# Performance work log

Measured on AMD Instinct MI355X. Metric: run time of the kernel, lower is better.

The kernel has to match this reference:

```python
import jax, jax.numpy as jnp
import numpy as np

EPS = 1e-8


def _conv1(x, w):
    # x: [C,H,W], w: [O,C,k,k] -> [O,H,W] (SAME padding, stride 1)
    return jax.lax.conv_general_dilated(
        x[None], w, window_strides=(1, 1), padding='SAME',
        dimension_numbers=('NCHW', 'OIHW', 'NCHW'))[0]


def setup_inputs() -> dict:
    key = jax.random.key(0)
    k1, k2, k3, k4 = jax.random.split(key, 4)
    B, C, O, K, S, H, W = 8, 512, 512, 3, 512, 64, 64
    inp = jax.random.normal(k1, (B, C, H, W), dtype=jnp.float32)
    style = jax.random.normal(k2, (B, S), dtype=jnp.float32)
    weight = jax.random.normal(k3, (1, O, C, K, K), dtype=jnp.float32)  # conv weight
    mod_weight = jax.random.normal(k4, (C, S), dtype=jnp.float32)      # EqualLinear weight
    mod_bias = jnp.ones((C,), dtype=jnp.float32)                        # bias filled with 1.0
    return {"input": inp, "style": style, "weight": weight,
            "mod_weight": mod_weight, "mod_bias": mod_bias}


def reference(input, style, weight, mod_weight, mod_bias) -> jnp.ndarray:
    B, C, H, W = input.shape
    _, O, _, K, _ = weight.shape
    fan_in = C * K * K
    scale = 1.0 / np.sqrt(fan_in)
    lin_scale = 1.0 / np.sqrt(mod_weight.shape[1])

    # EqualLinear modulation: [B, C]
    s = style @ (mod_weight * lin_scale).T + mod_bias

    # Modulate + demodulate per-sample weights: [B, O, C, K, K]
    w = scale * weight * s[:, None, :, None, None]
    demod = jax.lax.rsqrt(jnp.sum(w * w, axis=(2, 3, 4)) + EPS)  # [B, O]
    w = w * demod[:, :, None, None, None]

    # Grouped conv with groups=B == per-sample conv, vmapped over batch
    out = jax.vmap(_conv1)(input, w)  # [B, O, H, W]
    return out
```

## Files before the change

kernel.cpp:

```cpp
#include <hip/hip_runtime.h>

typedef unsigned short u16;
typedef __bf16 bf16_t;
typedef bf16_t bf16x8 __attribute__((ext_vector_type(8)));
typedef float floatx4 __attribute__((ext_vector_type(4)));

static constexpr float kScale = 0.014731391274719741f;
static constexpr float kScale2 = 2.1701388888888894e-4f;
static constexpr float kLinScale = 0.044194173824159216f;

__device__ __forceinline__ u16 f2bf(float f) {
  unsigned u = __float_as_uint(f);
  u += 0x7FFFu + ((u >> 16) & 1u);
  return (u16)(u >> 16);
}

#define GLD16(g, l)                                                        \
  __builtin_amdgcn_global_load_lds(                                        \
      (const __attribute__((address_space(1))) unsigned int*)(g),          \
      (__attribute__((address_space(3))) unsigned int*)(l), 16, 0, 0)

__global__ __launch_bounds__(256) void k_prep1(const float* __restrict__ style,
                                               const float* __restrict__ modw,
                                               const float* __restrict__ modb,
                                               const float* __restrict__ weight,
                                               float* __restrict__ s_buf,
                                               float* __restrict__ ssq) {
  int tid = threadIdx.x;
  if (blockIdx.x < 1024) {
    int lane = tid & 63, wv = tid >> 6;
    int idx = blockIdx.x * 4 + wv;
    int b = idx >> 9, c = idx & 511;
    const float* st = style + b * 512;
    const float* mw = modw + (size_t)c * 512;
    float s = 0.f;
#pragma unroll
    for (int i = 0; i < 8; ++i) s += st[lane + i * 64] * mw[lane + i * 64];
#pragma unroll
    for (int off = 32; off; off >>= 1) s += __shfl_xor(s, off);
    if (lane == 0) s_buf[idx] = s * kLinScale + modb[c];
  } else {
    int e = (blockIdx.x - 1024) * 256 + tid;
    const float* wp = weight + (size_t)e * 9;
    float ss = 0.f;
#pragma unroll
    for (int t = 0; t < 9; ++t) ss += wp[t] * wp[t];
    ssq[e] = ss;
  }
}

__global__ __launch_bounds__(256) void k_demod2(const float* __restrict__ ssq,
                                                const float* __restrict__ s_buf,
                                                float* __restrict__ demod_buf) {
  int tid = threadIdx.x, lane = tid & 63, wv = tid >> 6;
  int idx = blockIdx.x * 4 + wv;
  int b = idx >> 9, o = idx & 511;
  const float* sq = ssq + (size_t)o * 512;
  const float* srow = s_buf + b * 512;
  float ss = 0.f;
#pragma unroll
  for (int i = 0; i < 8; ++i) {
    float s = srow[lane + i * 64];
    ss += sq[lane + i * 64] * s * s;
  }
#pragma unroll
  for (int off = 32; off; off >>= 1) ss += __shfl_xor(ss, off);
  if (lane == 0) demod_buf[idx] = rsqrtf(ss * kScale2 + 1e-8f);
}

__global__ __launch_bounds__(256) void k_transpose(const float* __restrict__ in,
                                                   const float* __restrict__ s_buf,
                                                   unsigned* __restrict__ in_t32) {
  __shared__ u16 tile[64 * 65];
  int tid = threadIdx.x;
  int c0 = blockIdx.x * 64, y = blockIdx.y, b = blockIdx.z;
  const float* src = in + ((size_t)(b * 512 + c0) * 4096) + y * 64;
  const float* srow = s_buf + b * 512 + c0;
#pragma unroll
  for (int it = 0; it < 16; ++it) {
    int idx = it * 256 + tid;
    int cl = idx >> 6, x = idx & 63;
    tile[cl * 65 + x] = f2bf(src[(size_t)cl * 4096 + x] * srow[cl]);
  }
  __syncthreads();
  unsigned* dst = in_t32 + ((size_t)(b * 64 + y) * 64) * 256 + (c0 >> 1);
#pragma unroll
  for (int it = 0; it < 8; ++it) {
    int flat = it * 256 + tid;
    int cl2 = flat & 31, x = flat >> 5;
    unsigned lo = tile[(2 * cl2) * 65 + x];
    unsigned hi = tile[(2 * cl2 + 1) * 65 + x];
    dst[(size_t)x * 256 + cl2] = lo | (hi << 16);
  }
}

__global__ __launch_bounds__(256) void k_wfrag(const float* __restrict__ weight,
                                               unsigned* __restrict__ wt32) {
  __shared__ u16 tiles[9][512];
  int tid = threadIdx.x;
  int ct = blockIdx.x, ot = blockIdx.y;
  int o0 = ot * 16, c0 = ct * 32;
#pragma unroll
  for (int i = 0; i < 18; ++i) {
    int flat = i * 256 + tid;
    int t9 = flat / 9;
    int tap = flat - t9 * 9;
    int o_l = t9 >> 5, c_l = t9 & 31;
    float w = weight[((size_t)(o0 + o_l) * 512 + c0 + c_l) * 9 + tap];
    int pos = ((o_l + ((c_l >> 3) << 4)) << 3) + (c_l & 7);
    tiles[tap][pos] = f2bf(w * kScale);
  }
  __syncthreads();
  const unsigned* tl = (const unsigned*)tiles;
#pragma unroll
  for (int tap = 0; tap < 9; ++tap)
    wt32[(size_t)((tap * 16 + ct) * 32 + ot) * 256 + tid] = tl[tap * 256 + tid];
}

__global__ __launch_bounds__(256, 2) void k_conv(const u16* __restrict__ in_t,
                                                 const u16* __restrict__ w_t,
                                                 const float* __restrict__ demod_buf,
                                                 float* __restrict__ out) {
  __shared__ char smem[67584];
  const int tid = threadIdx.x;
  const int lane = tid & 63;
  const int wv = tid >> 6;
  const int wm = wv >> 1, wn = wv & 1;
  const int quad = lane >> 4, m16 = lane & 15;
  const int lin = blockIdx.x + 32 * blockIdx.y + 128 * blockIdx.z;
  const int b = lin & 7;
  const int r_ = lin >> 3;
  const int nt = r_ & 31;
  const int mt = r_ >> 5;
  const int y0 = nt * 2;

  floatx4 acc[4][4];
#pragma unroll
  for (int i = 0; i < 4; ++i)
#pragma unroll
    for (int j = 0; j < 4; ++j) acc[i][j] = (floatx4){0.f, 0.f, 0.f, 0.f};

  const u16* abase = w_t + mt * 4096 + wm * 2048 + lane * 8;

  const int xs = tid >> 3, qs = tid & 7;
  const int cch = qs ^ (xs & 7);
  const u16* gB[4];
  bool rok[4];
#pragma unroll
  for (int r = 0; r < 4; ++r) {
    int y = y0 - 1 + r;
    rok[r] = (unsigned)y < 64u;
    gB[r] = in_t + (((size_t)(b * 64 + (rok[r] ? y : 0)) * 64 + xs) * 512 + cch * 8);
  }

  char* bA[6];
#pragma unroll
  for (int dx = 0; dx < 3; ++dx) {
    const int sx0 = m16 + dx - 1;
#pragma unroll
    for (int kh = 0; kh < 2; ++kh)
      bA[dx * 2 + kh] = smem + wn * 8448 + (sx0 + 1) * 128 +
                        (((kh * 4 + quad) ^ (sx0 & 7)) << 4);
  }

  bf16x8 aR[2][2][4];
  bf16x8 bv[2][2][4];

#define LOAD_BV(si, bufimm, t_)                                              \
  {                                                                          \
    const int dy_ = (t_) / 3, dx_ = (t_) % 3;                                \
    _Pragma("unroll") for (int kh = 0; kh < 2; ++kh)                         \
      _Pragma("unroll") for (int ns = 0; ns < 4; ++ns)                       \
        bv[si][kh][ns] = *(const bf16x8*)(bA[dx_ * 2 + kh] + (bufimm) +      \
                                          dy_ * 8448 + ns * 2048);           \
  }

#define STAGE_B(bufimm)                                                      \
  {                                                                          \
    _Pragma("unroll") for (int r = 0; r < 4; ++r)                            \
      if (rok[r]) {                                                          \
        GLD16(gB[r], smem + (bufimm) + r * 8448 + 128 + wv * 1024);          \
        GLD16(gB[r] + 16384,                                                 \
              smem + (bufimm) + r * 8448 + 128 + 4096 + wv * 1024);          \
      }                                                                      \
  }

#define LOAD_A2(si, tp_, ctp_)                                               \
  {                                                                          \
    _Pragma("unroll") for (int kh = 0; kh < 2; ++kh) {                       \
      const u16* ap_ =                                                       \
          abase + ((size_t)((tp_)*16 + 2 * (ctp_) + kh) << 14);              \
      _Pragma("unroll") for (int ms = 0; ms < 4; ++ms)                       \
        aR[si][kh][ms] = *(const bf16x8*)(ap_ + ms * 512);                   \
    }                                                                        \
  }

#define CT_BODY(ctv, par, CURIMM, NXTIMM)                                    \
  {                                                                          \
    LOAD_BV(par, CURIMM, 0);                                                 \
    if ((ctv) + 1 < 8) {                                                     \
      _Pragma("unroll") for (int r = 0; r < 4; ++r) gB[r] += 64;             \
      STAGE_B(NXTIMM);                                                       \
    }                                                                        \
    _Pragma("unroll") for (int t = 0; t < 9; ++t) {                          \
      const int icur = (t + (par)) & 1;                                      \
      const int inxt = icur ^ 1;                                             \
      const int tp = t < 8 ? t + 1 : 0;                                      \
      const int ctp = t < 8 ? (ctv) : (ctv) + 1;                             \
      LOAD_A2(inxt, tp, ctp);                                                \
      if (t < 8) { LOAD_BV(inxt, CURIMM, t + 1); }                           \
      __builtin_amdgcn_s_setprio(1);                                         \
      _Pragma("unroll") for (int kh = 0; kh < 2; ++kh)                       \
        _Pragma("unroll") for (int ns = 0; ns < 4; ++ns)                     \
          _Pragma("unroll") for (int ms = 0; ms < 4; ++ms)                   \
            acc[ms][ns] = __builtin_amdgcn_mfma_f32_16x16x32_bf16(           \
                aR[icur][kh][ms], bv[icur][kh][ns], acc[ms][ns], 0, 0, 0);   \
      __builtin_amdgcn_s_setprio(0);                                         \
    }                                                                        \
    asm volatile("s_waitcnt vmcnt(8)" ::: "memory");                         \
    __builtin_amdgcn_s_barrier();                                            \
  }

  {
    const uint4 z = make_uint4(0u, 0u, 0u, 0u);
    for (int i = tid; i < 4224; i += 256) ((uint4*)smem)[i] = z;
  }
  __syncthreads();
  STAGE_B(0);
  __syncthreads();
  LOAD_A2(0, 0, 0);

  for (int ct = 0; ct < 8; ct += 2) {
    CT_BODY(ct, 0, 0, 33792);
    CT_BODY(ct + 1, 1, 33792, 0);
  }

#undef LOAD_BV
#undef STAGE_B
#undef LOAD_A2
#undef CT_BODY

  const int ob = mt * 128 + wm * 64;
  const int nb = nt * 128 + wn * 64;
#pragma unroll
  for (int ms = 0; ms < 4; ++ms)
#pragma unroll
    for (int ns = 0; ns < 4; ++ns) {
      const int n = nb + ns * 16 + m16;
#pragma unroll
      for (int r = 0; r < 4; ++r) {
        const int o = ob + ms * 16 + quad * 4 + r;
        float dm = demod_buf[b * 512 + o];
        out[((size_t)(b * 512 + o) << 12) + n] = acc[ms][ns][r] * dm;
      }
    }
}

extern "C" void kernel_launch(void* const* d_in, const int* in_sizes, int n_in,
                              void* d_out, int out_size, void* d_ws, size_t ws_size,
                              hipStream_t stream) {
  const float* input = (const float*)d_in[0];
  const float* style = (const float*)d_in[1];
  const float* weight = (const float*)d_in[2];
  const float* modw = (const float*)d_in[3];
  const float* modb = (const float*)d_in[4];
  float* out = (float*)d_out;
  char* ws = (char*)d_ws;
  float* s_buf = (float*)ws;
  float* demod_buf = (float*)(ws + 16384);
  float* ssq = (float*)(ws + 32768);
  u16* in_t = (u16*)(ws + 32768 + 1048576);
  u16* w_t = (u16*)(ws + 32768 + 1048576 + 33554432);

  k_prep1<<<dim3(2048), dim3(256), 0, stream>>>(style, modw, modb, weight, s_buf, ssq);
  k_demod2<<<dim3(1024), dim3(256), 0, stream>>>(ssq, s_buf, demod_buf);
  k_transpose<<<dim3(8, 64, 8), dim3(256), 0, stream>>>(input, s_buf, (unsigned*)in_t);
  k_wfrag<<<dim3(16, 32), dim3(256), 0, stream>>>(weight, (unsigned*)w_t);
  k_conv<<<dim3(32, 4, 8), dim3(256), 0, stream>>>(in_t, w_t, demod_buf, out);
}
```

Before: 249.3 us.

## Switch conv MFMA from 16x16x32 to 32x32x16 tiles with matching fragment layouts

```diff
diff --git a/kernel.cpp b/kernel.cpp
--- a/kernel.cpp
+++ b/kernel.cpp
@@ -4,6 +4,7 @@
 typedef __bf16 bf16_t;
 typedef bf16_t bf16x8 __attribute__((ext_vector_type(8)));
 typedef float floatx4 __attribute__((ext_vector_type(4)));
+typedef float floatx16 __attribute__((ext_vector_type(16)));
 
 static constexpr float kScale = 0.014731391274719741f;
 static constexpr float kScale2 = 2.1701388888888894e-4f;
@@ -96,25 +97,26 @@
 
 __global__ __launch_bounds__(256) void k_wfrag(const float* __restrict__ weight,
                                                unsigned* __restrict__ wt32) {
-  __shared__ u16 tiles[9][512];
   int tid = threadIdx.x;
-  int ct = blockIdx.x, ot = blockIdx.y;
-  int o0 = ot * 16, c0 = ct * 32;
-#pragma unroll
-  for (int i = 0; i < 18; ++i) {
-    int flat = i * 256 + tid;
-    int t9 = flat / 9;
-    int tap = flat - t9 * 9;
-    int o_l = t9 >> 5, c_l = t9 & 31;
-    float w = weight[((size_t)(o0 + o_l) * 512 + c0 + c_l) * 9 + tap];
-    int pos = ((o_l + ((c_l >> 3) << 4)) << 3) + (c_l & 7);
-    tiles[tap][pos] = f2bf(w * kScale);
-  }
-  __syncthreads();
-  const unsigned* tl = (const unsigned*)tiles;
-#pragma unroll
-  for (int tap = 0; tap < 9; ++tap)
-    wt32[(size_t)((tap * 16 + ct) * 32 + ot) * 256 + tid] = tl[tap * 256 + tid];
+  int ct8 = blockIdx.x;
+  int ot = blockIdx.y;
+#pragma unroll
+  for (int tap = 0; tap < 9; ++tap) {
+#pragma unroll
+    for (int i = 0; i < 4; ++i) {
+      int f32i = i * 256 + tid;
+      int ks = f32i >> 8;
+      int rem = f32i & 255;
+      int lane = rem >> 2;
+      int ep = (rem & 3) * 2;
+      int o = ot * 32 + (lane & 31);
+      int c = ct8 * 64 + ks * 16 + (lane >> 5) * 8 + ep;
+      unsigned lo = f2bf(weight[((size_t)o * 512 + c) * 9 + tap] * kScale);
+      unsigned hi = f2bf(weight[((size_t)o * 512 + c + 1) * 9 + tap] * kScale);
+      wt32[((size_t)(((tap * 8 + ct8) * 16 + ot) * 4 + ks) << 8) + rem] =
+          lo | (hi << 16);
+    }
+  }
 }
 
 __global__ __launch_bounds__(256, 2) void k_conv(const u16* __restrict__ in_t,
@@ -126,7 +128,7 @@
   const int lane = tid & 63;
   const int wv = tid >> 6;
   const int wm = wv >> 1, wn = wv & 1;
-  const int quad = lane >> 4, m16 = lane & 15;
+  const int n31 = lane & 31, h = lane >> 5;
   const int lin = blockIdx.x + 32 * blockIdx.y + 128 * blockIdx.z;
   const int b = lin & 7;
   const int r_ = lin >> 3;
@@ -134,13 +136,13 @@
   const int mt = r_ >> 5;
   const int y0 = nt * 2;
 
-  floatx4 acc[4][4];
-#pragma unroll
-  for (int i = 0; i < 4; ++i)
-#pragma unroll
-    for (int j = 0; j < 4; ++j) acc[i][j] = (floatx4){0.f, 0.f, 0.f, 0.f};
-
-  const u16* abase = w_t + mt * 4096 + wm * 2048 + lane * 8;
+  floatx16 acc[2][2];
+#pragma unroll
+  for (int i = 0; i < 2; ++i)
+#pragma unroll
+    for (int j = 0; j < 2; ++j)
+#pragma unroll
+      for (int r = 0; r < 16; ++r) acc[i][j][r] = 0.f;
 
   const int xs = tid >> 3, qs = tid & 7;
   const int cch = qs ^ (xs & 7);
@@ -153,15 +155,7 @@
     gB[r] = in_t + (((size_t)(b * 64 + (rok[r] ? y : 0)) * 64 + xs) * 512 + cch * 8);
   }
 
-  char* bA[6];
-#pragma unroll
-  for (int dx = 0; dx < 3; ++dx) {
-    const int sx0 = m16 + dx - 1;
-#pragma unroll
-    for (int kh = 0; kh < 2; ++kh)
-      bA[dx * 2 + kh] = smem + wn * 8448 + (sx0 + 1) * 128 +
-                        (((kh * 4 + quad) ^ (sx0 & 7)) << 4);
-  }
+  const int wnrow = wn * 8448;
 
   bf16x8 aR[2][2][4];
   bf16x8 bv[2][2][4];
@@ -169,10 +163,14 @@
 #define LOAD_BV(si, bufimm, t_)                                              \
   {                                                                          \
     const int dy_ = (t_) / 3, dx_ = (t_) % 3;                                \
-    _Pragma("unroll") for (int kh = 0; kh < 2; ++kh)                         \
-      _Pragma("unroll") for (int ns = 0; ns < 4; ++ns)                       \
-        bv[si][kh][ns] = *(const bf16x8*)(bA[dx_ * 2 + kh] + (bufimm) +      \
-                                          dy_ * 8448 + ns * 2048);           \
+    _Pragma("unroll") for (int n2 = 0; n2 < 2; ++n2) {                       \
+      const int sx = n2 * 32 + n31 + dx_ - 1;                                \
+      char* base_ = smem + (bufimm) + wnrow + dy_ * 8448 + (sx + 1) * 128 +  \
+                    ((h ^ (sx & 1)) << 4);                                   \
+      const int T_ = (sx & 6) << 4;                                          \
+      _Pragma("unroll") for (int ks = 0; ks < 4; ++ks)                       \
+        bv[si][n2][ks] = *(const bf16x8*)(base_ + ((ks << 5) ^ T_));         \
+    }                                                                        \
   }
 
 #define STAGE_B(bufimm)                                                      \
@@ -187,11 +185,13 @@
 
 #define LOAD_A2(si, tp_, ctp_)                                               \
   {                                                                          \
-    _Pragma("unroll") for (int kh = 0; kh < 2; ++kh) {                       \
+    _Pragma("unroll") for (int mt2 = 0; mt2 < 2; ++mt2) {                    \
       const u16* ap_ =                                                       \
-          abase + ((size_t)((tp_)*16 + 2 * (ctp_) + kh) << 14);              \
-      _Pragma("unroll") for (int ms = 0; ms < 4; ++ms)                       \
-        aR[si][kh][ms] = *(const bf16x8*)(ap_ + ms * 512);                   \
+          w_t +                                                              \
+          ((size_t)(((tp_)*8 + (ctp_)) * 16 + (mt * 4 + wm * 2 + mt2)) << 11) + \
+          lane * 8;                                                          \
+      _Pragma("unroll") for (int ks = 0; ks < 4; ++ks)                       \
+        aR[si][mt2][ks] = *(const bf16x8*)(ap_ + ks * 512);                  \
     }                                                                        \
   }
 
@@ -206,15 +206,16 @@
       const int icur = (t + (par)) & 1;                                      \
       const int inxt = icur ^ 1;                                             \
       const int tp = t < 8 ? t + 1 : 0;                                      \
-      const int ctp = t < 8 ? (ctv) : (ctv) + 1;                             \
+      const int ctp = t < 8 ? (ctv) : (((ctv) + 1) & 7);                     \
       LOAD_A2(inxt, tp, ctp);                                                \
       if (t < 8) { LOAD_BV(inxt, CURIMM, t + 1); }                           \
       __builtin_amdgcn_s_setprio(1);                                         \
-      _Pragma("unroll") for (int kh = 0; kh < 2; ++kh)                       \
-        _Pragma("unroll") for (int ns = 0; ns < 4; ++ns)                     \
-          _Pragma("unroll") for (int ms = 0; ms < 4; ++ms)                   \
-            acc[ms][ns] = __builtin_amdgcn_mfma_f32_16x16x32_bf16(           \
-                aR[icur][kh][ms], bv[icur][kh][ns], acc[ms][ns], 0, 0, 0);   \
+      _Pragma("unroll") for (int ks = 0; ks < 4; ++ks)                       \
+        _Pragma("unroll") for (int mt2 = 0; mt2 < 2; ++mt2)                  \
+          _Pragma("unroll") for (int nt2 = 0; nt2 < 2; ++nt2)                \
+            acc[mt2][nt2] = __builtin_amdgcn_mfma_f32_32x32x16_bf16(         \
+                aR[icur][mt2][ks], bv[icur][nt2][ks], acc[mt2][nt2],         \
+                0, 0, 0);                                                    \
       __builtin_amdgcn_s_setprio(0);                                         \
     }                                                                        \
     asm volatile("s_waitcnt vmcnt(8)" ::: "memory");                         \
@@ -240,18 +241,18 @@
 #undef LOAD_A2
 #undef CT_BODY
 
-  const int ob = mt * 128 + wm * 64;
-  const int nb = nt * 128 + wn * 64;
-#pragma unroll
-  for (int ms = 0; ms < 4; ++ms)
-#pragma unroll
-    for (int ns = 0; ns < 4; ++ns) {
-      const int n = nb + ns * 16 + m16;
-#pragma unroll
-      for (int r = 0; r < 4; ++r) {
-        const int o = ob + ms * 16 + quad * 4 + r;
+#pragma unroll
+  for (int mt2 = 0; mt2 < 2; ++mt2)
+#pragma unroll
+    for (int nt2 = 0; nt2 < 2; ++nt2) {
+      const int x = nt2 * 32 + n31;
+      const int ybase = (y0 + wn) * 64 + x;
+#pragma unroll
+      for (int r = 0; r < 16; ++r) {
+        const int o = mt * 128 + wm * 64 + mt2 * 32 +
+                      (r & 3) + 8 * (r >> 2) + 4 * h;
         float dm = demod_buf[b * 512 + o];
-        out[((size_t)(b * 512 + o) << 12) + n] = acc[ms][ns][r] * dm;
+        out[((size_t)(b * 512 + o) << 12) + ybase] = acc[mt2][nt2][r] * dm;
       }
     }
 }
@@ -275,6 +276,6 @@
   k_prep1<<<dim3(2048), dim3(256), 0, stream>>>(style, modw, modb, weight, s_buf, ssq);
   k_demod2<<<dim3(1024), dim3(256), 0, stream>>>(ssq, s_buf, demod_buf);
   k_transpose<<<dim3(8, 64, 8), dim3(256), 0, stream>>>(input, s_buf, (unsigned*)in_t);
-  k_wfrag<<<dim3(16, 32), dim3(256), 0, stream>>>(weight, (unsigned*)w_t);
+  k_wfrag<<<dim3(8, 16), dim3(256), 0, stream>>>(weight, (unsigned*)w_t);
   k_conv<<<dim3(32, 4, 8), dim3(256), 0, stream>>>(in_t, w_t, demod_buf, out);
 }
```

New measurement: 321.2 us. 1.29x slower.
